# Kernel optimization log

Measured on AMD Instinct MI355X. Metric: run time of the kernel, lower is better.

## Reference

```python
import jax, jax.numpy as jnp
import numpy as np

B, S, H, OUT = 4096, 200, 512, 64


def setup_inputs() -> dict:
    key = jax.random.key(0)
    ks = jax.random.split(key, 16)
    sc = 0.05
    return {
        "last_input": jax.random.normal(ks[0], (B, OUT), jnp.float32),
        "hidden": jax.random.normal(ks[1], (1, B, H), jnp.float32),
        "encoder_outputs": jax.random.normal(ks[2], (S, B, H), jnp.float32),
        "attn_W": jax.random.normal(ks[3], (S, H + OUT), jnp.float32) * sc,
        "attn_b": jax.random.normal(ks[4], (S,), jnp.float32) * sc,
        "comb_W": jax.random.normal(ks[5], (H, H + OUT), jnp.float32) * sc,
        "comb_b": jax.random.normal(ks[6], (H,), jnp.float32) * sc,
        "w_ih": jax.random.normal(ks[7], (3 * H, H), jnp.float32) * sc,
        "w_hh": jax.random.normal(ks[8], (3 * H, H), jnp.float32) * sc,
        "b_ih": jax.random.normal(ks[9], (3 * H,), jnp.float32) * sc,
        "b_hh": jax.random.normal(ks[10], (3 * H,), jnp.float32) * sc,
        "out_W": jax.random.normal(ks[11], (OUT, H), jnp.float32) * sc,
        "out_b": jax.random.normal(ks[12], (OUT,), jnp.float32) * sc,
    }


def reference(last_input, hidden, encoder_outputs, attn_W, attn_b, comb_W,
              comb_b, w_ih, w_hh, b_ih, b_hh, out_W, out_b):
    h0 = hidden[0]  # [B,H]
    # Bahdanau-style attention scores over the encoder sequence
    cat1 = jnp.concatenate([last_input, h0], axis=1)          # [B, OUT+H]
    attn_weights = jax.nn.softmax(cat1 @ attn_W.T + attn_b, axis=1)  # [B,S]
    enc = jnp.transpose(encoder_outputs, (1, 0, 2))            # [B,S,H]
    attn_applied = jnp.einsum('bs,bsh->bh', attn_weights, enc)  # [B,H]
    # combine + relu
    cat2 = jnp.concatenate([last_input, attn_applied], axis=1)  # [B, OUT+H]
    x = jax.nn.relu(cat2 @ comb_W.T + comb_b)                   # [B,H]
    # single-step GRU (PyTorch gate order: r, z, n)
    gi = x @ w_ih.T + b_ih                                      # [B,3H]
    gh = h0 @ w_hh.T + b_hh                                     # [B,3H]
    i_r, i_z, i_n = jnp.split(gi, 3, axis=1)
    h_r, h_z, h_n = jnp.split(gh, 3, axis=1)
    r = jax.nn.sigmoid(i_r + h_r)
    z = jax.nn.sigmoid(i_z + h_z)
    n = jnp.tanh(i_n + r * h_n)
    h_new = (1.0 - z) * n + z * h0                              # [B,H]
    out = h_new @ out_W.T + out_b                               # [B,OUT]
    return out, h_new[None], attn_weights
```

## Files before the change

### kernel.cpp

```cpp
#include <hip/hip_runtime.h>
#include <cstddef>

constexpr int Bn = 4096;
constexpr int Sn = 200;
constexpr int Hn = 512;
constexpr int On = 64;
constexpr int K1 = 576;

constexpr size_t HNEW_OFF = (size_t)Bn * On;
constexpr size_t AW_OFF   = (size_t)Bn * On + (size_t)Bn * Hn;

constexpr size_t CAT1B_OFF = 0;
constexpr size_t CAT2B_OFF = CAT1B_OFF + (size_t)Bn * K1 * 2;
constexpr size_t XB_OFF    = CAT2B_OFF + (size_t)Bn * K1 * 2;
constexpr size_t WIHB_OFF  = XB_OFF    + (size_t)Bn * Hn * 2;
constexpr size_t WHHB_OFF  = WIHB_OFF  + (size_t)3 * Hn * Hn * 2;
constexpr size_t CWB_OFF   = WHHB_OFF  + (size_t)3 * Hn * Hn * 2;
constexpr size_t OWB_OFF   = CWB_OFF   + (size_t)Hn * K1 * 2;
constexpr size_t AWB_OFF   = OWB_OFF   + (size_t)On * Hn * 2;
constexpr size_t HNB_OFF   = AWB_OFF   + (size_t)256 * K1 * 2;

typedef __attribute__((ext_vector_type(8))) short bf16x8;
typedef __attribute__((ext_vector_type(4))) float f32x4;

__device__ __forceinline__ float sigmoidf_(float v) { return 1.f / (1.f + __expf(-v)); }
__device__ __forceinline__ unsigned short f2bf(float f) {
    unsigned u = __float_as_uint(f);
    return (unsigned short)((u + 0x7FFFu + ((u >> 16) & 1u)) >> 16);
}
__device__ __forceinline__ ushort4 pack4(float4 v) {
    ushort4 o = { f2bf(v.x), f2bf(v.y), f2bf(v.z), f2bf(v.w) };
    return o;
}

__global__ __launch_bounds__(256) void cvt_all_kernel(
    const float* __restrict__ hidden, const float* __restrict__ wih,
    const float* __restrict__ whh, const float* __restrict__ combW,
    const float* __restrict__ outW, const float* __restrict__ attnW,
    const float* __restrict__ li,
    unsigned short* __restrict__ cat1b, unsigned short* __restrict__ cat2b,
    unsigned short* __restrict__ wihb, unsigned short* __restrict__ whhb,
    unsigned short* __restrict__ combWb, unsigned short* __restrict__ outWb,
    unsigned short* __restrict__ awWb)
{
    const int blk = blockIdx.x;
    const int t = threadIdx.x;
    if (blk < 2048) {
        size_t off = (size_t)blk * 1024 + (size_t)t * 4;
        int b = (int)(off >> 9), col = (int)(off & 511);
        float4 v = *(const float4*)(hidden + off);
        *(ushort4*)(cat1b + (size_t)b * K1 + On + col) = pack4(v);
    } else if (blk < 3584) {
        size_t off = (size_t)(blk - 2048) * 1024 + (size_t)t * 4;
        const float* s = (blk < 2816) ? wih : whh;
        unsigned short* d = (blk < 2816) ? wihb : whhb;
        if (blk >= 2816) off -= (size_t)768 * 1024;
        float4 v = *(const float4*)(s + off);
        *(ushort4*)(d + off) = pack4(v);
    } else if (blk < 3872) {
        size_t off = (size_t)(blk - 3584) * 1024 + (size_t)t * 4;
        float4 v = *(const float4*)(combW + off);
        *(ushort4*)(combWb + off) = pack4(v);
    } else if (blk < 3904) {
        size_t off = (size_t)(blk - 3872) * 1024 + (size_t)t * 4;
        float4 v = *(const float4*)(outW + off);
        *(ushort4*)(outWb + off) = pack4(v);
    } else if (blk < 4017) {
        size_t off = (size_t)(blk - 3904) * 1024 + (size_t)t * 4;
        if (off < (size_t)Sn * K1) {
            float4 v = *(const float4*)(attnW + off);
            *(ushort4*)(awWb + off) = pack4(v);
        }
    } else if (blk < 4049) {
        size_t off = (size_t)Sn * K1 + (size_t)(blk - 4017) * 1024 + (size_t)t * 4;
        if (off < (size_t)256 * K1) {
            ushort4 z = {0, 0, 0, 0};
            *(ushort4*)(awWb + off) = z;
        }
    } else {
        size_t off = (size_t)(blk - 4049) * 1024 + (size_t)t * 4;
        int b = (int)(off >> 6), col = (int)(off & 63);
        float4 v = *(const float4*)(li + off);
        ushort4 o = pack4(v);
        *(ushort4*)(cat1b + (size_t)b * K1 + col) = o;
        *(ushort4*)(cat2b + (size_t)b * K1 + col) = o;
    }
}

template<int MF, int NF, bool RELU, bool OUT_BF16>
__device__ __forceinline__ void gemm_bt_body(
    const unsigned short* __restrict__ A, int lda,
    const unsigned short* __restrict__ B,
    const float* __restrict__ bias, float* __restrict__ Cf,
    unsigned short* __restrict__ Cb, int K, int ldc,
    int m0, int n0, int nmax)
{
    constexpr int BM = 32 * MF;
    constexpr int BN = 32 * NF;
    __shared__ unsigned short As[BM * 64];
    __shared__ unsigned short Bs[BN * 64];

    const int tid = threadIdx.x;
    const int wave = tid >> 6;
    const int lane = tid & 63;
    const int wm = wave >> 1, wn = wave & 1;
    const int l15 = lane & 15, lg = lane >> 4;

    f32x4 acc[MF][NF];
#pragma unroll
    for (int i = 0; i < MF; ++i)
#pragma unroll
        for (int j = 0; j < NF; ++j) acc[i][j] = (f32x4){0.f, 0.f, 0.f, 0.f};

    for (int kc = 0; kc < K; kc += 64) {
        __syncthreads();
#pragma unroll
        for (int i = 0; i < BM * 8 / 256; ++i) {
            int idx = tid + i * 256;
            int row = idx >> 3, ck = idx & 7;
            uint4 v = *(const uint4*)(A + (size_t)(m0 + row) * lda + kc + ck * 8);
            int byte = row * 128 + ((ck * 16) ^ ((row & 7) << 4));
            *(uint4*)((char*)As + byte) = v;
        }
#pragma unroll
        for (int i = 0; i < BN * 8 / 256; ++i) {
            int idx = tid + i * 256;
            int row = idx >> 3, ck = idx & 7;
            uint4 v = *(const uint4*)(B + (size_t)(n0 + row) * K + kc + ck * 8);
            int byte = row * 128 + ((ck * 16) ^ ((row & 7) << 4));
            *(uint4*)((char*)Bs + byte) = v;
        }
        __syncthreads();
#pragma unroll
        for (int s = 0; s < 2; ++s) {
            bf16x8 af[MF], bfr[NF];
#pragma unroll
            for (int i = 0; i < MF; ++i) {
                int row = wm * (MF * 16) + i * 16 + l15;
                int byte = row * 128 + ((s * 64 + lg * 16) ^ ((row & 7) << 4));
                af[i] = *(const bf16x8*)((const char*)As + byte);
            }
#pragma unroll
            for (int j = 0; j < NF; ++j) {
                int row = wn * (NF * 16) + j * 16 + l15;
                int byte = row * 128 + ((s * 64 + lg * 16) ^ ((row & 7) << 4));
                bfr[j] = *(const bf16x8*)((const char*)Bs + byte);
            }
#pragma unroll
            for (int i = 0; i < MF; ++i)
#pragma unroll
                for (int j = 0; j < NF; ++j)
                    acc[i][j] = __builtin_amdgcn_mfma_f32_16x16x32_bf16(
                        af[i], bfr[j], acc[i][j], 0, 0, 0);
        }
    }

#pragma unroll
    for (int i = 0; i < MF; ++i) {
        int m = m0 + wm * (MF * 16) + i * 16 + lg * 4;
#pragma unroll
        for (int j = 0; j < NF; ++j) {
            int n = n0 + wn * (NF * 16) + j * 16 + l15;
            if (n < nmax) {
                float bv = bias[n];
#pragma unroll
                for (int r = 0; r < 4; ++r) {
                    float v = acc[i][j][r] + bv;
                    if (RELU) v = fmaxf(v, 0.f);
                    if (OUT_BF16) Cb[(size_t)(m + r) * ldc + n] = f2bf(v);
                    else          Cf[(size_t)(m + r) * ldc + n] = v;
                }
            }
        }
    }
}

__global__ __launch_bounds__(256, 2) void comb_gemm_kernel(
    const unsigned short* __restrict__ cat2b, const unsigned short* __restrict__ combWb,
    const float* __restrict__ comb_b, unsigned short* __restrict__ xb)
{
    gemm_bt_body<4, 4, true, true>(cat2b, K1, combWb, comb_b, nullptr, xb,
                                   K1, Hn, blockIdx.x * 128, blockIdx.y * 128, Hn);
}

__global__ __launch_bounds__(256, 2) void out_gemm_kernel(
    const unsigned short* __restrict__ hnewb, const unsigned short* __restrict__ outWb,
    const float* __restrict__ out_b, float* __restrict__ dout)
{
    gemm_bt_body<4, 2, false, false>(hnewb, Hn, outWb, out_b, dout, nullptr,
                                     Hn, On, blockIdx.x * 128, 0, On);
}

__global__ __launch_bounds__(256) void scores_softmax_kernel(
    const unsigned short* __restrict__ cat1b, const unsigned short* __restrict__ awWb,
    const float* __restrict__ attn_b, float* __restrict__ dout)
{
    __shared__ unsigned short As[64 * 64];
    __shared__ unsigned short Bs[256 * 64];
    __shared__ float smax[4][64];
    __shared__ float ssum[4][64];

    const int tid = threadIdx.x;
    const int m0 = blockIdx.x * 64;
    const int wave = tid >> 6;
    const int lane = tid & 63;
    const int l15 = lane & 15, lg = lane >> 4;

    f32x4 acc[4][4];
#pragma unroll
    for (int i = 0; i < 4; ++i)
#pragma unroll
        for (int j = 0; j < 4; ++j) acc[i][j] = (f32x4){0.f, 0.f, 0.f, 0.f};

    for (int kc = 0; kc < K1; kc += 64) {
        __syncthreads();
#pragma unroll
        for (int i = 0; i < 2; ++i) {
            int idx = tid + i * 256;
            int row = idx >> 3, ck = idx & 7;
            uint4 v = *(const uint4*)(cat1b + (size_t)(m0 + row) * K1 + kc + ck * 8);
            int byte = row * 128 + ((ck * 16) ^ ((row & 7) << 4));
            *(uint4*)((char*)As + byte) = v;
        }
#pragma unroll
        for (int i = 0; i < 8; ++i) {
            int idx = tid + i * 256;
            int row = idx >> 3, ck = idx & 7;
            uint4 v = *(const uint4*)(awWb + (size_t)row * K1 + kc + ck * 8);
            int byte = row * 128 + ((ck * 16) ^ ((row & 7) << 4));
            *(uint4*)((char*)Bs + byte) = v;
        }
        __syncthreads();
#pragma unroll
        for (int s = 0; s < 2; ++s) {
            bf16x8 af[4], bfr[4];
#pragma unroll
            for (int i = 0; i < 4; ++i) {
                int row = i * 16 + l15;
                int byte = row * 128 + ((s * 64 + lg * 16) ^ ((row & 7) << 4));
                af[i] = *(const bf16x8*)((const char*)As + byte);
            }
#pragma unroll
            for (int j = 0; j < 4; ++j) {
                int row = wave * 64 + j * 16 + l15;
                int byte = row * 128 + ((s * 64 + lg * 16) ^ ((row & 7) << 4));
                bfr[j] = *(const bf16x8*)((const char*)Bs + byte);
            }
#pragma unroll
            for (int i = 0; i < 4; ++i)
#pragma unroll
                for (int j = 0; j < 4; ++j)
                    acc[i][j] = __builtin_amdgcn_mfma_f32_16x16x32_bf16(
                        af[i], bfr[j], acc[i][j], 0, 0, 0);
        }
    }

#pragma unroll
    for (int i = 0; i < 4; ++i)
#pragma unroll
        for (int j = 0; j < 4; ++j) {
            int n = wave * 64 + j * 16 + l15;
            float bv = (n < Sn) ? attn_b[n] : 0.f;
#pragma unroll
            for (int r = 0; r < 4; ++r)
                acc[i][j][r] = (n < Sn) ? (acc[i][j][r] + bv) : -3.0e38f;
        }

#pragma unroll
    for (int i = 0; i < 4; ++i) {
#pragma unroll
        for (int r = 0; r < 4; ++r) {
            float mx = fmaxf(fmaxf(acc[i][0][r], acc[i][1][r]),
                             fmaxf(acc[i][2][r], acc[i][3][r]));
#pragma unroll
            for (int o = 8; o > 0; o >>= 1) mx = fmaxf(mx, __shfl_xor(mx, o, 64));
            if (l15 == 0) smax[wave][i * 16 + lg * 4 + r] = mx;
        }
    }
    __syncthreads();
#pragma unroll
    for (int i = 0; i < 4; ++i) {
#pragma unroll
        for (int r = 0; r < 4; ++r) {
            int row = i * 16 + lg * 4 + r;
            float mx = fmaxf(fmaxf(smax[0][row], smax[1][row]),
                             fmaxf(smax[2][row], smax[3][row]));
            float sum = 0.f;
#pragma unroll
            for (int j = 0; j < 4; ++j) {
                float e = __expf(acc[i][j][r] - mx);
                acc[i][j][r] = e;
                sum += e;
            }
#pragma unroll
            for (int o = 8; o > 0; o >>= 1) sum += __shfl_xor(sum, o, 64);
            if (l15 == 0) ssum[wave][row] = sum;
        }
    }
    __syncthreads();
#pragma unroll
    for (int i = 0; i < 4; ++i) {
#pragma unroll
        for (int r = 0; r < 4; ++r) {
            int row = i * 16 + lg * 4 + r;
            float inv = 1.f / (ssum[0][row] + ssum[1][row] + ssum[2][row] + ssum[3][row]);
#pragma unroll
            for (int j = 0; j < 4; ++j) {
                int n = wave * 64 + j * 16 + l15;
                if (n < Sn)
                    dout[AW_OFF + (size_t)(m0 + row) * Sn + n] = acc[i][j][r] * inv;
            }
        }
    }
}

__global__ __launch_bounds__(256) void attn_apply_kernel(
    const float* __restrict__ enc, const float* __restrict__ aw,
    unsigned short* __restrict__ cat2b)
{
    __shared__ float wl[2 * Sn];
    const int tid = threadIdx.x;
    const int b0 = blockIdx.x * 2;

    for (int idx = tid; idx < 2 * Sn; idx += 256)
        wl[idx] = aw[(size_t)b0 * Sn + idx];
    __syncthreads();

    const int r = tid >> 7;
    const int hc = tid & 127;
    const f32x4* base = (const f32x4*)enc + ((size_t)(b0 + r)) * 128 + hc;
    const float* w = &wl[r * Sn];

    f32x4 acc = {0, 0, 0, 0};
#pragma unroll 4
    for (int s = 0; s < Sn; ++s) {
        f32x4 v = __builtin_nontemporal_load(base + (size_t)s * (Bn * 128));
        acc += v * w[s];
    }

    ushort4 o = { f2bf(acc[0]), f2bf(acc[1]), f2bf(acc[2]), f2bf(acc[3]) };
    *(ushort4*)(cat2b + (size_t)(b0 + r) * K1 + On + hc * 4) = o;
}

__device__ __forceinline__ void gru_gemm_phase(
    const unsigned short* __restrict__ A, int lda,
    const unsigned short* __restrict__ W,
    int m0, int n0, int tid, int wm, int wn, int l15, int lg,
    unsigned short* As, unsigned short* Bs,
    f32x4 aR[2][2], f32x4 aZ[2][2], f32x4 aN[2][2])
{
    for (int kc = 0; kc < Hn; kc += 64) {
        __syncthreads();
#pragma unroll
        for (int i = 0; i < 2; ++i) {
            int idx = tid + i * 256;
            int row = idx >> 3, ck = idx & 7;
            uint4 v = *(const uint4*)(A + (size_t)(m0 + row) * lda + kc + ck * 8);
            int byte = row * 128 + ((ck * 16) ^ ((row & 7) << 4));
            *(uint4*)((char*)As + byte) = v;
        }
#pragma unroll
        for (int g = 0; g < 3; ++g)
#pragma unroll
            for (int i = 0; i < 2; ++i) {
                int idx = tid + i * 256;
                int row = idx >> 3, ck = idx & 7;
                uint4 v = *(const uint4*)(W + (size_t)(g * Hn + n0 + row) * Hn + kc + ck * 8);
                int byte = row * 128 + ((ck * 16) ^ ((row & 7) << 4));
                *(uint4*)((char*)Bs + g * 8192 + byte) = v;
            }
        __syncthreads();
#pragma unroll
        for (int s = 0; s < 2; ++s) {
            bf16x8 af[2], bf0[2], bf1[2], bf2[2];
#pragma unroll
            for (int i = 0; i < 2; ++i) {
                int row = wm * 32 + i * 16 + l15;
                int byte = row * 128 + ((s * 64 + lg * 16) ^ ((row & 7) << 4));
                af[i] = *(const bf16x8*)((const char*)As + byte);
            }
#pragma unroll
            for (int j = 0; j < 2; ++j) {
                int row = wn * 32 + j * 16 + l15;
                int byte = row * 128 + ((s * 64 + lg * 16) ^ ((row & 7) << 4));
                bf0[j] = *(const bf16x8*)((const char*)Bs + 0 * 8192 + byte);
                bf1[j] = *(const bf16x8*)((const char*)Bs + 1 * 8192 + byte);
                bf2[j] = *(const bf16x8*)((const char*)Bs + 2 * 8192 + byte);
            }
#pragma unroll
            for (int i = 0; i < 2; ++i)
#pragma unroll
                for (int j = 0; j < 2; ++j) {
                    aR[i][j] = __builtin_amdgcn_mfma_f32_16x16x32_bf16(af[i], bf0[j], aR[i][j], 0, 0, 0);
                    aZ[i][j] = __builtin_amdgcn_mfma_f32_16x16x32_bf16(af[i], bf1[j], aZ[i][j], 0, 0, 0);
                    aN[i][j] = __builtin_amdgcn_mfma_f32_16x16x32_bf16(af[i], bf2[j], aN[i][j], 0, 0, 0);
                }
        }
    }
}

__global__ __launch_bounds__(256, 2) void gru_fused_kernel(
    const unsigned short* __restrict__ xb, const unsigned short* __restrict__ cat1b,
    const unsigned short* __restrict__ wihb, const unsigned short* __restrict__ whhb,
    const float* __restrict__ b_ih, const float* __restrict__ b_hh,
    const float* __restrict__ hidden,
    float* __restrict__ dout, unsigned short* __restrict__ hnewb)
{
    __shared__ unsigned short As[64 * 64];
    __shared__ unsigned short Bs[3 * 64 * 64];

    const int tid = threadIdx.x;
    const int m0 = blockIdx.x * 64;
    const int n0 = blockIdx.y * 64;
    const int wave = tid >> 6, lane = tid & 63;
    const int wm = wave >> 1, wn = wave & 1;
    const int l15 = lane & 15, lg = lane >> 4;

    f32x4 aR[2][2], aZ[2][2], aN0[2][2], aN1[2][2];
#pragma unroll
    for (int i = 0; i < 2; ++i)
#pragma unroll
        for (int j = 0; j < 2; ++j) {
            aR[i][j] = (f32x4){0.f, 0.f, 0.f, 0.f};
            aZ[i][j] = (f32x4){0.f, 0.f, 0.f, 0.f};
            aN0[i][j] = (f32x4){0.f, 0.f, 0.f, 0.f};
            aN1[i][j] = (f32x4){0.f, 0.f, 0.f, 0.f};
        }

    gru_gemm_phase(xb, Hn, wihb, m0, n0, tid, wm, wn, l15, lg, As, Bs, aR, aZ, aN0);
    gru_gemm_phase(cat1b + On, K1, whhb, m0, n0, tid, wm, wn, l15, lg, As, Bs, aR, aZ, aN1);

#pragma unroll
    for (int j = 0; j < 2; ++j) {
        const int n = n0 + wn * 32 + j * 16 + l15;
        const float bR = b_ih[n] + b_hh[n];
        const float bZ = b_ih[Hn + n] + b_hh[Hn + n];
        const float bI = b_ih[2 * Hn + n];
        const float bH = b_hh[2 * Hn + n];
#pragma unroll
        for (int i = 0; i < 2; ++i) {
            const int mb = m0 + wm * 32 + i * 16 + lg * 4;
#pragma unroll
            for (int r = 0; r < 4; ++r) {
                const int m = mb + r;
                float h0 = hidden[(size_t)m * Hn + n];
                float rg = sigmoidf_(aR[i][j][r] + bR);
                float zg = sigmoidf_(aZ[i][j][r] + bZ);
                float ng = tanhf(aN0[i][j][r] + bI + rg * (aN1[i][j][r] + bH));
                float o = (1.f - zg) * ng + zg * h0;
                dout[HNEW_OFF + (size_t)m * Hn + n] = o;
                hnewb[(size_t)m * Hn + n] = f2bf(o);
            }
        }
    }
}

extern "C" void kernel_launch(void* const* d_in, const int* in_sizes, int n_in,
                              void* d_out, int out_size, void* d_ws, size_t ws_size,
                              hipStream_t stream)
{
    const float* last_input = (const float*)d_in[0];
    const float* hidden     = (const float*)d_in[1];
    const float* enc        = (const float*)d_in[2];
    const float* attn_W     = (const float*)d_in[3];
    const float* attn_b     = (const float*)d_in[4];
    const float* comb_W     = (const float*)d_in[5];
    const float* comb_b     = (const float*)d_in[6];
    const float* w_ih       = (const float*)d_in[7];
    const float* w_hh       = (const float*)d_in[8];
    const float* b_ih       = (const float*)d_in[9];
    const float* b_hh       = (const float*)d_in[10];
    const float* out_W      = (const float*)d_in[11];
    const float* out_b      = (const float*)d_in[12];

    float* out = (float*)d_out;
    char*  ws  = (char*)d_ws;
    unsigned short* cat1b  = (unsigned short*)(ws + CAT1B_OFF);
    unsigned short* cat2b  = (unsigned short*)(ws + CAT2B_OFF);
    unsigned short* xb     = (unsigned short*)(ws + XB_OFF);
    unsigned short* wihb   = (unsigned short*)(ws + WIHB_OFF);
    unsigned short* whhb   = (unsigned short*)(ws + WHHB_OFF);
    unsigned short* combWb = (unsigned short*)(ws + CWB_OFF);
    unsigned short* outWb  = (unsigned short*)(ws + OWB_OFF);
    unsigned short* awWb   = (unsigned short*)(ws + AWB_OFF);
    unsigned short* hnewb  = (unsigned short*)(ws + HNB_OFF);

    cvt_all_kernel<<<4305, 256, 0, stream>>>(hidden, w_ih, w_hh, comb_W, out_W,
                                             attn_W, last_input,
                                             cat1b, cat2b, wihb, whhb, combWb,
                                             outWb, awWb);
    scores_softmax_kernel<<<Bn / 64, 256, 0, stream>>>(cat1b, awWb, attn_b, out);
    attn_apply_kernel<<<Bn / 2, 256, 0, stream>>>(enc, out + AW_OFF, cat2b);
    comb_gemm_kernel<<<dim3(Bn / 128, Hn / 128), 256, 0, stream>>>(cat2b, combWb, comb_b, xb);
    gru_fused_kernel<<<dim3(Bn / 64, Hn / 64), 256, 0, stream>>>(
        xb, cat1b, wihb, whhb, b_ih, b_hh, hidden, out, hnewb);
    out_gemm_kernel<<<Bn / 128, 256, 0, stream>>>(hnewb, outWb, out_b, out);
}
```

Measured before the change: 374.6 us.

## Split scores GEMM from softmax and process four batch rows per attn_apply block

Result: faster. 359.4 us (-4.0%).

```diff
diff --git a/kernel.cpp b/kernel.cpp
--- a/kernel.cpp
+++ b/kernel.cpp
@@ -18,7 +18,8 @@
 constexpr size_t CWB_OFF   = WHHB_OFF  + (size_t)3 * Hn * Hn * 2;
 constexpr size_t OWB_OFF   = CWB_OFF   + (size_t)Hn * K1 * 2;
 constexpr size_t AWB_OFF   = OWB_OFF   + (size_t)On * Hn * 2;
-constexpr size_t HNB_OFF   = AWB_OFF   + (size_t)256 * K1 * 2;
+constexpr size_t LOG_OFF   = AWB_OFF   + (size_t)256 * K1 * 2;
+constexpr size_t HNB_OFF   = LOG_OFF   + (size_t)Bn * Sn * 4;
 
 typedef __attribute__((ext_vector_type(8))) short bf16x8;
 typedef __attribute__((ext_vector_type(4))) float f32x4;
@@ -175,6 +176,14 @@
     }
 }
 
+__global__ __launch_bounds__(256, 2) void scores_gemm_kernel(
+    const unsigned short* __restrict__ cat1b, const unsigned short* __restrict__ awWb,
+    const float* __restrict__ attn_b, float* __restrict__ logits)
+{
+    gemm_bt_body<2, 2, false, false>(cat1b, K1, awWb, attn_b, logits, nullptr,
+                                     K1, Sn, blockIdx.x * 64, blockIdx.y * 64, Sn);
+}
+
 __global__ __launch_bounds__(256, 2) void comb_gemm_kernel(
     const unsigned short* __restrict__ cat2b, const unsigned short* __restrict__ combWb,
     const float* __restrict__ comb_b, unsigned short* __restrict__ xb)
@@ -191,126 +200,36 @@
                                      Hn, On, blockIdx.x * 128, 0, On);
 }
 
-__global__ __launch_bounds__(256) void scores_softmax_kernel(
-    const unsigned short* __restrict__ cat1b, const unsigned short* __restrict__ awWb,
-    const float* __restrict__ attn_b, float* __restrict__ dout)
-{
-    __shared__ unsigned short As[64 * 64];
-    __shared__ unsigned short Bs[256 * 64];
-    __shared__ float smax[4][64];
-    __shared__ float ssum[4][64];
-
-    const int tid = threadIdx.x;
-    const int m0 = blockIdx.x * 64;
-    const int wave = tid >> 6;
-    const int lane = tid & 63;
-    const int l15 = lane & 15, lg = lane >> 4;
-
-    f32x4 acc[4][4];
-#pragma unroll
-    for (int i = 0; i < 4; ++i)
-#pragma unroll
-        for (int j = 0; j < 4; ++j) acc[i][j] = (f32x4){0.f, 0.f, 0.f, 0.f};
-
-    for (int kc = 0; kc < K1; kc += 64) {
-        __syncthreads();
-#pragma unroll
-        for (int i = 0; i < 2; ++i) {
-            int idx = tid + i * 256;
-            int row = idx >> 3, ck = idx & 7;
-            uint4 v = *(const uint4*)(cat1b + (size_t)(m0 + row) * K1 + kc + ck * 8);
-            int byte = row * 128 + ((ck * 16) ^ ((row & 7) << 4));
-            *(uint4*)((char*)As + byte) = v;
-        }
-#pragma unroll
-        for (int i = 0; i < 8; ++i) {
-            int idx = tid + i * 256;
-            int row = idx >> 3, ck = idx & 7;
-            uint4 v = *(const uint4*)(awWb + (size_t)row * K1 + kc + ck * 8);
-            int byte = row * 128 + ((ck * 16) ^ ((row & 7) << 4));
-            *(uint4*)((char*)Bs + byte) = v;
-        }
-        __syncthreads();
-#pragma unroll
-        for (int s = 0; s < 2; ++s) {
-            bf16x8 af[4], bfr[4];
-#pragma unroll
-            for (int i = 0; i < 4; ++i) {
-                int row = i * 16 + l15;
-                int byte = row * 128 + ((s * 64 + lg * 16) ^ ((row & 7) << 4));
-                af[i] = *(const bf16x8*)((const char*)As + byte);
-            }
-#pragma unroll
-            for (int j = 0; j < 4; ++j) {
-                int row = wave * 64 + j * 16 + l15;
-                int byte = row * 128 + ((s * 64 + lg * 16) ^ ((row & 7) << 4));
-                bfr[j] = *(const bf16x8*)((const char*)Bs + byte);
-            }
-#pragma unroll
-            for (int i = 0; i < 4; ++i)
-#pragma unroll
-                for (int j = 0; j < 4; ++j)
-                    acc[i][j] = __builtin_amdgcn_mfma_f32_16x16x32_bf16(
-                        af[i], bfr[j], acc[i][j], 0, 0, 0);
-        }
-    }
-
-#pragma unroll
-    for (int i = 0; i < 4; ++i)
-#pragma unroll
-        for (int j = 0; j < 4; ++j) {
-            int n = wave * 64 + j * 16 + l15;
-            float bv = (n < Sn) ? attn_b[n] : 0.f;
-#pragma unroll
-            for (int r = 0; r < 4; ++r)
-                acc[i][j][r] = (n < Sn) ? (acc[i][j][r] + bv) : -3.0e38f;
-        }
-
-#pragma unroll
-    for (int i = 0; i < 4; ++i) {
-#pragma unroll
-        for (int r = 0; r < 4; ++r) {
-            float mx = fmaxf(fmaxf(acc[i][0][r], acc[i][1][r]),
-                             fmaxf(acc[i][2][r], acc[i][3][r]));
-#pragma unroll
-            for (int o = 8; o > 0; o >>= 1) mx = fmaxf(mx, __shfl_xor(mx, o, 64));
-            if (l15 == 0) smax[wave][i * 16 + lg * 4 + r] = mx;
-        }
-    }
-    __syncthreads();
-#pragma unroll
-    for (int i = 0; i < 4; ++i) {
-#pragma unroll
-        for (int r = 0; r < 4; ++r) {
-            int row = i * 16 + lg * 4 + r;
-            float mx = fmaxf(fmaxf(smax[0][row], smax[1][row]),
-                             fmaxf(smax[2][row], smax[3][row]));
-            float sum = 0.f;
-#pragma unroll
-            for (int j = 0; j < 4; ++j) {
-                float e = __expf(acc[i][j][r] - mx);
-                acc[i][j][r] = e;
-                sum += e;
-            }
-#pragma unroll
-            for (int o = 8; o > 0; o >>= 1) sum += __shfl_xor(sum, o, 64);
-            if (l15 == 0) ssum[wave][row] = sum;
-        }
-    }
-    __syncthreads();
-#pragma unroll
-    for (int i = 0; i < 4; ++i) {
-#pragma unroll
-        for (int r = 0; r < 4; ++r) {
-            int row = i * 16 + lg * 4 + r;
-            float inv = 1.f / (ssum[0][row] + ssum[1][row] + ssum[2][row] + ssum[3][row]);
-#pragma unroll
-            for (int j = 0; j < 4; ++j) {
-                int n = wave * 64 + j * 16 + l15;
-                if (n < Sn)
-                    dout[AW_OFF + (size_t)(m0 + row) * Sn + n] = acc[i][j][r] * inv;
-            }
-        }
+__global__ __launch_bounds__(256) void softmax_kernel(
+    const float* __restrict__ logits, float* __restrict__ dout)
+{
+    const int row = blockIdx.x * 4 + (threadIdx.x >> 6);
+    const int lane = threadIdx.x & 63;
+    const float* lp = logits + (size_t)row * Sn;
+    float v[4], e[4];
+    float m = -3.0e38f;
+#pragma unroll
+    for (int k = 0; k < 4; ++k) {
+        int s = lane + 64 * k;
+        v[k] = (s < Sn) ? lp[s] : -3.0e38f;
+        m = fmaxf(m, v[k]);
+    }
+#pragma unroll
+    for (int o = 32; o > 0; o >>= 1) m = fmaxf(m, __shfl_xor(m, o, 64));
+    float sum = 0.f;
+#pragma unroll
+    for (int k = 0; k < 4; ++k) {
+        int s = lane + 64 * k;
+        e[k] = (s < Sn) ? __expf(v[k] - m) : 0.f;
+        sum += e[k];
+    }
+#pragma unroll
+    for (int o = 32; o > 0; o >>= 1) sum += __shfl_xor(sum, o, 64);
+    float inv = 1.f / sum;
+#pragma unroll
+    for (int k = 0; k < 4; ++k) {
+        int s = lane + 64 * k;
+        if (s < Sn) dout[AW_OFF + (size_t)row * Sn + s] = e[k] * inv;
     }
 }
 
@@ -318,28 +237,35 @@
     const float* __restrict__ enc, const float* __restrict__ aw,
     unsigned short* __restrict__ cat2b)
 {
-    __shared__ float wl[2 * Sn];
+    __shared__ float wl[4 * Sn];
     const int tid = threadIdx.x;
-    const int b0 = blockIdx.x * 2;
-
-    for (int idx = tid; idx < 2 * Sn; idx += 256)
+    const int b0 = blockIdx.x * 4;
+
+    for (int idx = tid; idx < 4 * Sn; idx += 256)
         wl[idx] = aw[(size_t)b0 * Sn + idx];
     __syncthreads();
 
-    const int r = tid >> 7;
+    const int q = tid >> 7;
     const int hc = tid & 127;
-    const f32x4* base = (const f32x4*)enc + ((size_t)(b0 + r)) * 128 + hc;
-    const float* w = &wl[r * Sn];
-
-    f32x4 acc = {0, 0, 0, 0};
-#pragma unroll 4
+    const f32x4* base = (const f32x4*)enc + ((size_t)(b0 + q * 2)) * 128 + hc;
+
+    f32x4 a0 = {0, 0, 0, 0}, a1 = {0, 0, 0, 0};
+
+#pragma unroll 2
     for (int s = 0; s < Sn; ++s) {
-        f32x4 v = __builtin_nontemporal_load(base + (size_t)s * (Bn * 128));
-        acc += v * w[s];
-    }
-
-    ushort4 o = { f2bf(acc[0]), f2bf(acc[1]), f2bf(acc[2]), f2bf(acc[3]) };
-    *(ushort4*)(cat2b + (size_t)(b0 + r) * K1 + On + hc * 4) = o;
+        const f32x4* p = base + (size_t)s * (Bn * 128);
+        f32x4 v0 = __builtin_nontemporal_load(p);
+        f32x4 v1 = __builtin_nontemporal_load(p + 128);
+        float w0 = wl[(q * 2 + 0) * Sn + s];
+        float w1 = wl[(q * 2 + 1) * Sn + s];
+        a0 += v0 * w0; a1 += v1 * w1;
+    }
+
+    const int h = hc * 4;
+    ushort4 o0 = { f2bf(a0[0]), f2bf(a0[1]), f2bf(a0[2]), f2bf(a0[3]) };
+    ushort4 o1 = { f2bf(a1[0]), f2bf(a1[1]), f2bf(a1[2]), f2bf(a1[3]) };
+    *(ushort4*)(cat2b + (size_t)(b0 + q * 2 + 0) * K1 + On + h) = o0;
+    *(ushort4*)(cat2b + (size_t)(b0 + q * 2 + 1) * K1 + On + h) = o1;
 }
 
 __device__ __forceinline__ void gru_gemm_phase(
@@ -483,14 +409,16 @@
     unsigned short* combWb = (unsigned short*)(ws + CWB_OFF);
     unsigned short* outWb  = (unsigned short*)(ws + OWB_OFF);
     unsigned short* awWb   = (unsigned short*)(ws + AWB_OFF);
+    float*          logits = (float*)(ws + LOG_OFF);
     unsigned short* hnewb  = (unsigned short*)(ws + HNB_OFF);
 
     cvt_all_kernel<<<4305, 256, 0, stream>>>(hidden, w_ih, w_hh, comb_W, out_W,
                                              attn_W, last_input,
                                              cat1b, cat2b, wihb, whhb, combWb,
                                              outWb, awWb);
-    scores_softmax_kernel<<<Bn / 64, 256, 0, stream>>>(cat1b, awWb, attn_b, out);
-    attn_apply_kernel<<<Bn / 2, 256, 0, stream>>>(enc, out + AW_OFF, cat2b);
+    scores_gemm_kernel<<<dim3(Bn / 64, 4), 256, 0, stream>>>(cat1b, awWb, attn_b, logits);
+    softmax_kernel<<<Bn / 4, 256, 0, stream>>>(logits, out);
+    attn_apply_kernel<<<Bn / 4, 256, 0, stream>>>(enc, out + AW_OFF, cat2b);
     comb_gemm_kernel<<<dim3(Bn / 128, Hn / 128), 256, 0, stream>>>(cat2b, combWb, comb_b, xb);
     gru_fused_kernel<<<dim3(Bn / 64, Hn / 64), 256, 0, stream>>>(
         xb, cat1b, wihb, whhb, b_ih, b_hh, hidden, out, hnewb);
```

## Overlap hidden-state GRU GEMM and weight conversion with attention-apply in one kernel

Applied to the files above, without the earlier changes.

After: 354.4 us. 5.4% less time.

```diff
diff --git a/kernel.cpp b/kernel.cpp
--- a/kernel.cpp
+++ b/kernel.cpp
@@ -18,7 +18,8 @@
 constexpr size_t CWB_OFF   = WHHB_OFF  + (size_t)3 * Hn * Hn * 2;
 constexpr size_t OWB_OFF   = CWB_OFF   + (size_t)Hn * K1 * 2;
 constexpr size_t AWB_OFF   = OWB_OFF   + (size_t)On * Hn * 2;
-constexpr size_t HNB_OFF   = AWB_OFF   + (size_t)256 * K1 * 2;
+constexpr size_t GHB_OFF   = AWB_OFF   + (size_t)256 * K1 * 2;
+constexpr size_t HNB_OFF   = GHB_OFF   + (size_t)Bn * 3 * Hn * 2;
 
 typedef __attribute__((ext_vector_type(8))) short bf16x8;
 typedef __attribute__((ext_vector_type(4))) float f32x4;
@@ -28,20 +29,19 @@
     unsigned u = __float_as_uint(f);
     return (unsigned short)((u + 0x7FFFu + ((u >> 16) & 1u)) >> 16);
 }
+__device__ __forceinline__ float bf2f(unsigned short b) {
+    return __uint_as_float((unsigned)b << 16);
+}
 __device__ __forceinline__ ushort4 pack4(float4 v) {
     ushort4 o = { f2bf(v.x), f2bf(v.y), f2bf(v.z), f2bf(v.w) };
     return o;
 }
 
-__global__ __launch_bounds__(256) void cvt_all_kernel(
-    const float* __restrict__ hidden, const float* __restrict__ wih,
-    const float* __restrict__ whh, const float* __restrict__ combW,
-    const float* __restrict__ outW, const float* __restrict__ attnW,
-    const float* __restrict__ li,
+__global__ __launch_bounds__(256) void cvt_min_kernel(
+    const float* __restrict__ hidden, const float* __restrict__ whh,
+    const float* __restrict__ attnW, const float* __restrict__ li,
     unsigned short* __restrict__ cat1b, unsigned short* __restrict__ cat2b,
-    unsigned short* __restrict__ wihb, unsigned short* __restrict__ whhb,
-    unsigned short* __restrict__ combWb, unsigned short* __restrict__ outWb,
-    unsigned short* __restrict__ awWb)
+    unsigned short* __restrict__ whhb, unsigned short* __restrict__ awWb)
 {
     const int blk = blockIdx.x;
     const int t = threadIdx.x;
@@ -50,35 +50,24 @@
         int b = (int)(off >> 9), col = (int)(off & 511);
         float4 v = *(const float4*)(hidden + off);
         *(ushort4*)(cat1b + (size_t)b * K1 + On + col) = pack4(v);
-    } else if (blk < 3584) {
+    } else if (blk < 2816) {
         size_t off = (size_t)(blk - 2048) * 1024 + (size_t)t * 4;
-        const float* s = (blk < 2816) ? wih : whh;
-        unsigned short* d = (blk < 2816) ? wihb : whhb;
-        if (blk >= 2816) off -= (size_t)768 * 1024;
-        float4 v = *(const float4*)(s + off);
-        *(ushort4*)(d + off) = pack4(v);
-    } else if (blk < 3872) {
-        size_t off = (size_t)(blk - 3584) * 1024 + (size_t)t * 4;
-        float4 v = *(const float4*)(combW + off);
-        *(ushort4*)(combWb + off) = pack4(v);
-    } else if (blk < 3904) {
-        size_t off = (size_t)(blk - 3872) * 1024 + (size_t)t * 4;
-        float4 v = *(const float4*)(outW + off);
-        *(ushort4*)(outWb + off) = pack4(v);
-    } else if (blk < 4017) {
-        size_t off = (size_t)(blk - 3904) * 1024 + (size_t)t * 4;
+        float4 v = *(const float4*)(whh + off);
+        *(ushort4*)(whhb + off) = pack4(v);
+    } else if (blk < 2929) {
+        size_t off = (size_t)(blk - 2816) * 1024 + (size_t)t * 4;
         if (off < (size_t)Sn * K1) {
             float4 v = *(const float4*)(attnW + off);
             *(ushort4*)(awWb + off) = pack4(v);
         }
-    } else if (blk < 4049) {
-        size_t off = (size_t)Sn * K1 + (size_t)(blk - 4017) * 1024 + (size_t)t * 4;
+    } else if (blk < 2961) {
+        size_t off = (size_t)Sn * K1 + (size_t)(blk - 2929) * 1024 + (size_t)t * 4;
         if (off < (size_t)256 * K1) {
             ushort4 z = {0, 0, 0, 0};
             *(ushort4*)(awWb + off) = z;
         }
     } else {
-        size_t off = (size_t)(blk - 4049) * 1024 + (size_t)t * 4;
+        size_t off = (size_t)(blk - 2961) * 1024 + (size_t)t * 4;
         int b = (int)(off >> 6), col = (int)(off & 63);
         float4 v = *(const float4*)(li + off);
         ushort4 o = pack4(v);
@@ -314,32 +303,76 @@
     }
 }
 
-__global__ __launch_bounds__(256) void attn_apply_kernel(
+__global__ __launch_bounds__(256, 2) void mega_kernel(
     const float* __restrict__ enc, const float* __restrict__ aw,
-    unsigned short* __restrict__ cat2b)
-{
-    __shared__ float wl[2 * Sn];
-    const int tid = threadIdx.x;
-    const int b0 = blockIdx.x * 2;
-
-    for (int idx = tid; idx < 2 * Sn; idx += 256)
-        wl[idx] = aw[(size_t)b0 * Sn + idx];
-    __syncthreads();
-
-    const int r = tid >> 7;
-    const int hc = tid & 127;
-    const f32x4* base = (const f32x4*)enc + ((size_t)(b0 + r)) * 128 + hc;
-    const float* w = &wl[r * Sn];
-
-    f32x4 acc = {0, 0, 0, 0};
-#pragma unroll 4
-    for (int s = 0; s < Sn; ++s) {
-        f32x4 v = __builtin_nontemporal_load(base + (size_t)s * (Bn * 128));
-        acc += v * w[s];
-    }
-
-    ushort4 o = { f2bf(acc[0]), f2bf(acc[1]), f2bf(acc[2]), f2bf(acc[3]) };
-    *(ushort4*)(cat2b + (size_t)(b0 + r) * K1 + On + hc * 4) = o;
+    unsigned short* __restrict__ cat2b,
+    const unsigned short* __restrict__ cat1b, const unsigned short* __restrict__ whhb,
+    const float* __restrict__ b_hh, unsigned short* __restrict__ ghb,
+    const float* __restrict__ wih, const float* __restrict__ combW,
+    const float* __restrict__ outW,
+    unsigned short* __restrict__ wihb, unsigned short* __restrict__ combWb,
+    unsigned short* __restrict__ outWb)
+{
+    const int blk = blockIdx.x;
+    if (blk < 512) {
+        __shared__ float wl[8 * Sn];
+        const int tid = threadIdx.x;
+        const int b0 = blk * 8;
+
+        for (int idx = tid; idx < 8 * Sn; idx += 256)
+            wl[idx] = aw[(size_t)b0 * Sn + idx];
+        __syncthreads();
+
+        const int q = tid >> 7;
+        const int hc = tid & 127;
+        const f32x4* base = (const f32x4*)enc + ((size_t)(b0 + q * 4)) * 128 + hc;
+
+        f32x4 a0 = {0,0,0,0}, a1 = {0,0,0,0}, a2 = {0,0,0,0}, a3 = {0,0,0,0};
+
+#pragma unroll 2
+        for (int s = 0; s < Sn; ++s) {
+            const f32x4* p = base + (size_t)s * (Bn * 128);
+            f32x4 v0 = __builtin_nontemporal_load(p);
+            f32x4 v1 = __builtin_nontemporal_load(p + 128);
+            f32x4 v2 = __builtin_nontemporal_load(p + 256);
+            f32x4 v3 = __builtin_nontemporal_load(p + 384);
+            float w0 = wl[(q * 4 + 0) * Sn + s];
+            float w1 = wl[(q * 4 + 1) * Sn + s];
+            float w2 = wl[(q * 4 + 2) * Sn + s];
+            float w3 = wl[(q * 4 + 3) * Sn + s];
+            a0 += v0 * w0; a1 += v1 * w1; a2 += v2 * w2; a3 += v3 * w3;
+        }
+
+        const int h = hc * 4;
+        f32x4 accs[4] = {a0, a1, a2, a3};
+#pragma unroll
+        for (int r = 0; r < 4; ++r) {
+            ushort4 o = { f2bf(accs[r][0]), f2bf(accs[r][1]), f2bf(accs[r][2]), f2bf(accs[r][3]) };
+            *(ushort4*)(cat2b + (size_t)(b0 + q * 4 + r) * K1 + On + h) = o;
+        }
+    } else if (blk < 896) {
+        const int qq = blk - 512;
+        const int m0 = (qq & 31) * 128;
+        const int n0 = (qq >> 5) * 128;
+        gemm_bt_body<4, 4, false, true>(cat1b + On, K1, whhb, b_hh, nullptr, ghb,
+                                        Hn, 3 * Hn, m0, n0, 3 * Hn);
+    } else {
+        const int r = blk - 896;
+        const int t = threadIdx.x;
+        if (r < 768) {
+            size_t off = (size_t)r * 1024 + (size_t)t * 4;
+            float4 v = *(const float4*)(wih + off);
+            *(ushort4*)(wihb + off) = pack4(v);
+        } else if (r < 1056) {
+            size_t off = (size_t)(r - 768) * 1024 + (size_t)t * 4;
+            float4 v = *(const float4*)(combW + off);
+            *(ushort4*)(combWb + off) = pack4(v);
+        } else {
+            size_t off = (size_t)(r - 1056) * 1024 + (size_t)t * 4;
+            float4 v = *(const float4*)(outW + off);
+            *(ushort4*)(outWb + off) = pack4(v);
+        }
+    }
 }
 
 __device__ __forceinline__ void gru_gemm_phase(
@@ -399,10 +432,9 @@
     }
 }
 
-__global__ __launch_bounds__(256, 2) void gru_fused_kernel(
-    const unsigned short* __restrict__ xb, const unsigned short* __restrict__ cat1b,
-    const unsigned short* __restrict__ wihb, const unsigned short* __restrict__ whhb,
-    const float* __restrict__ b_ih, const float* __restrict__ b_hh,
+__global__ __launch_bounds__(256, 2) void gru_gi_kernel(
+    const unsigned short* __restrict__ xb, const unsigned short* __restrict__ wihb,
+    const float* __restrict__ b_ih, const unsigned short* __restrict__ ghb,
     const float* __restrict__ hidden,
     float* __restrict__ dout, unsigned short* __restrict__ hnewb)
 {
@@ -416,37 +448,38 @@
     const int wm = wave >> 1, wn = wave & 1;
     const int l15 = lane & 15, lg = lane >> 4;
 
-    f32x4 aR[2][2], aZ[2][2], aN0[2][2], aN1[2][2];
+    f32x4 aR[2][2], aZ[2][2], aN[2][2];
 #pragma unroll
     for (int i = 0; i < 2; ++i)
 #pragma unroll
         for (int j = 0; j < 2; ++j) {
             aR[i][j] = (f32x4){0.f, 0.f, 0.f, 0.f};
             aZ[i][j] = (f32x4){0.f, 0.f, 0.f, 0.f};
-            aN0[i][j] = (f32x4){0.f, 0.f, 0.f, 0.f};
-            aN1[i][j] = (f32x4){0.f, 0.f, 0.f, 0.f};
-        }
-
-    gru_gemm_phase(xb, Hn, wihb, m0, n0, tid, wm, wn, l15, lg, As, Bs, aR, aZ, aN0);
-    gru_gemm_phase(cat1b + On, K1, whhb, m0, n0, tid, wm, wn, l15, lg, As, Bs, aR, aZ, aN1);
+            aN[i][j] = (f32x4){0.f, 0.f, 0.f, 0.f};
+        }
+
+    gru_gemm_phase(xb, Hn, wihb, m0, n0, tid, wm, wn, l15, lg, As, Bs, aR, aZ, aN);
 
 #pragma unroll
     for (int j = 0; j < 2; ++j) {
         const int n = n0 + wn * 32 + j * 16 + l15;
-        const float bR = b_ih[n] + b_hh[n];
-        const float bZ = b_ih[Hn + n] + b_hh[Hn + n];
+        const float bR = b_ih[n];
+        const float bZ = b_ih[Hn + n];
         const float bI = b_ih[2 * Hn + n];
-        const float bH = b_hh[2 * Hn + n];
 #pragma unroll
         for (int i = 0; i < 2; ++i) {
             const int mb = m0 + wm * 32 + i * 16 + lg * 4;
 #pragma unroll
             for (int r = 0; r < 4; ++r) {
                 const int m = mb + r;
-                float h0 = hidden[(size_t)m * Hn + n];
-                float rg = sigmoidf_(aR[i][j][r] + bR);
-                float zg = sigmoidf_(aZ[i][j][r] + bZ);
-                float ng = tanhf(aN0[i][j][r] + bI + rg * (aN1[i][j][r] + bH));
+                const unsigned short* gh = ghb + (size_t)m * (3 * Hn);
+                float h0  = hidden[(size_t)m * Hn + n];
+                float ghr = bf2f(gh[n]);
+                float ghz = bf2f(gh[Hn + n]);
+                float ghn = bf2f(gh[2 * Hn + n]);
+                float rg = sigmoidf_(aR[i][j][r] + bR + ghr);
+                float zg = sigmoidf_(aZ[i][j][r] + bZ + ghz);
+                float ng = tanhf(aN[i][j][r] + bI + rg * ghn);
                 float o = (1.f - zg) * ng + zg * h0;
                 dout[HNEW_OFF + (size_t)m * Hn + n] = o;
                 hnewb[(size_t)m * Hn + n] = f2bf(o);
@@ -483,16 +516,18 @@
     unsigned short* combWb = (unsigned short*)(ws + CWB_OFF);
     unsigned short* outWb  = (unsigned short*)(ws + OWB_OFF);
     unsigned short* awWb   = (unsigned short*)(ws + AWB_OFF);
+    unsigned short* ghb    = (unsigned short*)(ws + GHB_OFF);
     unsigned short* hnewb  = (unsigned short*)(ws + HNB_OFF);
 
-    cvt_all_kernel<<<4305, 256, 0, stream>>>(hidden, w_ih, w_hh, comb_W, out_W,
-                                             attn_W, last_input,
-                                             cat1b, cat2b, wihb, whhb, combWb,
-                                             outWb, awWb);
+    cvt_min_kernel<<<3217, 256, 0, stream>>>(hidden, w_hh, attn_W, last_input,
+                                             cat1b, cat2b, whhb, awWb);
     scores_softmax_kernel<<<Bn / 64, 256, 0, stream>>>(cat1b, awWb, attn_b, out);
-    attn_apply_kernel<<<Bn / 2, 256, 0, stream>>>(enc, out + AW_OFF, cat2b);
+    mega_kernel<<<1984, 256, 0, stream>>>(enc, out + AW_OFF, cat2b,
+                                          cat1b, whhb, b_hh, ghb,
+                                          w_ih, comb_W, out_W,
+                                          wihb, combWb, outWb);
     comb_gemm_kernel<<<dim3(Bn / 128, Hn / 128), 256, 0, stream>>>(cat2b, combWb, comb_b, xb);
-    gru_fused_kernel<<<dim3(Bn / 64, Hn / 64), 256, 0, stream>>>(
-        xb, cat1b, wihb, whhb, b_ih, b_hh, hidden, out, hnewb);
+    gru_gi_kernel<<<dim3(Bn / 64, Hn / 64), 256, 0, stream>>>(
+        xb, wihb, b_ih, ghb, hidden, out, hnewb);
     out_gemm_kernel<<<Bn / 128, 256, 0, stream>>>(hnewb, outWb, out_b, out);
 }
```
